# Performance work log

Hardware: AMD Instinct MI355X
Metric: run time of the kernel (lower is better)

Reference implementation:

```python
import jax, jax.numpy as jnp
import numpy as np

EPS = 1e-5   # torch F.layer_norm default eps
TOP_K = 20   # int(3*D^2 / (2*hr*N^2 + 10*D)) for D=768, N=196, hr=1.0
NUM_EXPERTS = 200  # 10 * TOP_K


def setup_inputs() -> dict:
    key = jax.random.key(0)
    ks = jax.random.split(key, 6)
    B, N, D = 32, 196, 768
    E, H = NUM_EXPERTS, 196  # H = int(N * hidden_ratio)
    s = 0.02
    return {
        "x": jax.random.normal(ks[0], (B, N, D), jnp.float32),
        "Wr": jax.random.normal(ks[1], (E, D), jnp.float32) * s,   # router.weight
        "W1": jax.random.normal(ks[2], (E, H, N), jnp.float32) * s,  # fc1.weight per expert
        "b1": jnp.zeros((E, H), jnp.float32),
        "W2": jax.random.normal(ks[3], (E, N, H), jnp.float32) * s,  # fc2.weight per expert
        "b2": jnp.zeros((E, N), jnp.float32),
        "Wo": jax.random.normal(ks[4], (D, D), jnp.float32) * s,     # out_proj.weight
        "bo": jnp.zeros((D,), jnp.float32),
    }


def reference(x, Wr, W1, b1, W2, b2, Wo, bo):
    B, N, D = x.shape
    E = Wr.shape[0]
    K = TOP_K

    # Router: per-sample routing on token-mean features
    logits = x.mean(axis=1) @ Wr.T                      # (B, E)
    probs = jax.nn.softmax(logits, axis=-1)             # (B, E)
    w, idx = jax.lax.top_k(probs, K)                    # (B, K) sorted desc, as torch.topk
    w = w / w.sum(axis=-1, keepdims=True)               # renormalize top-k weights

    # TokenMixer operates in (B, D, N) space: layernorm over tokens (no affine),
    # then fc1 (N->H), gelu(tanh), fc2 (H->N).
    xt = jnp.swapaxes(x, 1, 2)                          # (B, D, N)
    mu = xt.mean(axis=-1, keepdims=True)
    var = xt.var(axis=-1, keepdims=True)                # population var (matches F.layer_norm)
    z = (xt - mu) * jax.lax.rsqrt(var + EPS)            # (B, D, N)

    # Gather each sample's K expert weight matrices and batch the MLPs.
    W1g, b1g = W1[idx], b1[idx]                         # (B,K,H,N), (B,K,H)
    W2g, b2g = W2[idx], b2[idx]                         # (B,K,N,H), (B,K,N)

    h = jnp.einsum('bdn,bkhn->bkdh', z, W1g) + b1g[:, :, None, :]
    a = jax.nn.gelu(h, approximate=True)                # tanh-approx GELU
    o = jnp.einsum('bkdh,bknh->bkdn', a, W2g) + b2g[:, :, None, :]

    # Weighted combine over the K selected experts, back to (B, N, D)
    mix = jnp.einsum('bk,bkdn->bnd', w, o)

    out = mix @ Wo.T + bo                               # out_proj

    # Load-balancing aux loss (top-1 assignment fraction vs mean router prob)
    top1 = jax.nn.one_hot(idx[:, 0], E, dtype=probs.dtype)   # (B, E)
    aux = E * jnp.sum(probs.mean(axis=0) * top1.mean(axis=0))
    return out, aux
```

## Files before the change

kernel.cpp:

```cpp
#include <hip/hip_runtime.h>
#include <math.h>

constexpr int B  = 32;
constexpr int N  = 196;
constexpr int D  = 768;
constexpr int E  = 200;
constexpr int TK = 20;

constexpr int NGRP = 4;
constexpr int PRB  = 14336;
constexpr int EXB  = 114688;
constexpr int LK   = 40;

typedef __bf16 bf16x8 __attribute__((ext_vector_type(8)));
typedef __bf16 bf16x4 __attribute__((ext_vector_type(4)));
typedef float  f32x4  __attribute__((ext_vector_type(4)));
typedef long   longx2 __attribute__((ext_vector_type(2)));
typedef unsigned char uchar;

#define GLDS16(gp, lp)                                                        \
  __builtin_amdgcn_global_load_lds(                                           \
      (const __attribute__((address_space(1))) void*)(gp),                    \
      (__attribute__((address_space(3))) void*)(lp), 16, 0, 0)

#define WAITVM12  __builtin_amdgcn_s_waitcnt(0x0F7C)
#define WAITVM8   __builtin_amdgcn_s_waitcnt(0x0F78)
#define WAITVM0   __builtin_amdgcn_s_waitcnt(0x0F70)
#define WAITLGKM0 __builtin_amdgcn_s_waitcnt(0xC07F)
#define BAR       __builtin_amdgcn_s_barrier()

__device__ __forceinline__ float gelu_fast(float x) {
  float u = x * fmaf(x * x, 0.044715f, 1.0f);
  float e = exp2f(-2.3022084f * u);
  return x * __builtin_amdgcn_rcpf(1.0f + e);
}

__device__ __forceinline__ uchar f32_to_f8(float v) {
  return (uchar)(__builtin_amdgcn_cvt_pk_fp8_f32(v, v, 0, false) & 0xff);
}

__global__ __launch_bounds__(256) void k_ln(const float* __restrict__ x,
                                            uchar* __restrict__ zb,
                                            float* __restrict__ mu) {
  int b = blockIdx.x / 12, dt = blockIdx.x % 12;
  int d0 = dt * 64;
  int t = threadIdx.x;
  int q = t >> 6, d = t & 63;
  __shared__ float ps[256], pq[256];
  __shared__ float ms[64], rss[64];
  __shared__ alignas(16) uchar zt[64 * 256];

  for (int i = t; i < 1024; i += 256) ((uint4*)zt)[i] = (uint4){0, 0, 0, 0};

  const float* xp = x + ((size_t)b * N + q * 49) * D + d0 + d;
  float s = 0.f, sq = 0.f;
  #pragma unroll 7
  for (int n = 0; n < 49; ++n) {
    float v = xp[(size_t)n * D];
    s += v; sq += v * v;
  }
  ps[t] = s; pq[t] = sq;
  __syncthreads();
  if (t < 64) {
    float S = ps[t] + ps[t + 64] + ps[t + 128] + ps[t + 192];
    float Q = pq[t] + pq[t + 64] + pq[t + 128] + pq[t + 192];
    float m = S * (1.0f / N);
    float var = Q * (1.0f / N) - m * m;
    ms[t] = m; rss[t] = rsqrtf(var + 1e-5f);
    mu[(size_t)b * D + d0 + t] = m;
  }
  __syncthreads();
  float m = ms[d], r = rss[d];
  int dsw = (d >> 1) & 3;
  #pragma unroll 7
  for (int n = 0; n < 49; ++n) {
    float v = xp[(size_t)n * D];
    int tok = q * 49 + n;
    int qp = ((tok >> 3) & 3) ^ dsw;
    int off = d * 256 + (tok >> 6) * 64 + qp * 16 + ((tok >> 5) & 1) * 8 + (tok & 7);
    zt[off] = f32_to_f8((v - m) * r);
  }
  __syncthreads();
  #pragma unroll
  for (int pair = 0; pair < 4; ++pair) {
    uint4* dst = (uint4*)(zb + (((size_t)b * 4 + pair) * 768 + d0) * 64);
    dst[t] = ((const uint4*)zt)[(t >> 2) * 16 + pair * 4 + (t & 3)];
  }
}

__global__ __launch_bounds__(256) void k_convert(
    const float* __restrict__ W1, const float* __restrict__ W2,
    const float* __restrict__ Wo,
    uchar* __restrict__ Wf, __bf16* __restrict__ Wob) {
  int bx = blockIdx.x;
  int t = threadIdx.x;
  if (bx >= 400) {
    int i = (bx - 400) * 256 + t;
    float4 v = *(const float4*)&Wo[(size_t)i * 4];
    bf16x4 o = {(__bf16)v.x, (__bf16)v.y, (__bf16)v.z, (__bf16)v.w};
    *(bf16x4*)&Wob[(size_t)i * 4] = o;
    return;
  }
  int e = bx >> 1, mat = bx & 1;
  __shared__ alignas(16) uchar ls[224 * 256];
  for (int i = t; i < 3584; i += 256) ((uint4*)ls)[i] = (uint4){0, 0, 0, 0};
  __syncthreads();
  const float* src = (mat ? W2 : W1) + (size_t)e * 196 * 196;
  for (int i = t; i < 196 * 49; i += 256) {
    int r = i / 49, c4 = (i - r * 49) * 4;
    float4 v = *(const float4*)&src[(size_t)r * 196 + c4];
    int lo = __builtin_amdgcn_cvt_pk_fp8_f32(v.x, v.y, 0, false);
    unsigned int pk = (unsigned int)__builtin_amdgcn_cvt_pk_fp8_f32(v.z, v.w, lo, true);
    *(unsigned int*)&ls[r * 256 + c4] = pk;
  }
  __syncthreads();
  uchar* dst = Wf + (size_t)e * EXB + mat * 4 * PRB;
  for (int s = t; s < 3584; s += 256) {
    int p = s / 896, rem = s - p * 896;
    int col = rem >> 2, qp = rem & 3;
    int ql = qp ^ ((col >> 1) & 3);
    unsigned long lo = *(const unsigned long*)&ls[col * 256 + p * 64 + ql * 8];
    unsigned long hi = *(const unsigned long*)&ls[col * 256 + p * 64 + 32 + ql * 8];
    longx2 o; o[0] = (long)lo; o[1] = (long)hi;
    *(longx2*)&dst[(size_t)s * 16] = o;
  }
}

__global__ void k_router(const float* __restrict__ mu, const float* __restrict__ Wr,
                         float* __restrict__ probs, int* __restrict__ idxg,
                         float* __restrict__ wg) {
  int b = blockIdx.x;
  int t = threadIdx.x;
  __shared__ float smu[768];
  __shared__ float sp[E];
  __shared__ float smax, ssum;
  __shared__ float svals[TK];
  __shared__ int   sidx[TK];

  for (int i = t; i < 768; i += 256) smu[i] = mu[(size_t)b * D + i];
  __syncthreads();

  float logit = 0.f;
  if (t < E) {
    const float4* wr4 = (const float4*)(Wr + (size_t)t * D);
    const float4* m4  = (const float4*)smu;
    float acc = 0.f;
    #pragma unroll 4
    for (int i = 0; i < 192; ++i) {
      float4 w = wr4[i], m = m4[i];
      acc = fmaf(w.x, m.x, acc); acc = fmaf(w.y, m.y, acc);
      acc = fmaf(w.z, m.z, acc); acc = fmaf(w.w, m.w, acc);
    }
    logit = acc;
    sp[t] = acc;
  }
  __syncthreads();
  if (t == 0) {
    float mx = sp[0];
    for (int e = 1; e < E; ++e) mx = fmaxf(mx, sp[e]);
    smax = mx;
  }
  __syncthreads();
  if (t < E) sp[t] = expf(logit - smax);
  __syncthreads();
  if (t == 0) {
    float s = 0.f;
    for (int e = 0; e < E; ++e) s += sp[e];
    ssum = s;
  }
  __syncthreads();
  if (t < E) {
    sp[t] = sp[t] / ssum;
    probs[(size_t)b * E + t] = sp[t];
  }
  __syncthreads();

  for (int k = 0; k < TK; ++k) {
    if (t < 64) {
      float bv = -1e30f; int bi = 0;
      for (int e = t; e < E; e += 64) {
        float v = sp[e];
        if (v > bv) { bv = v; bi = e; }
      }
      #pragma unroll
      for (int off = 32; off > 0; off >>= 1) {
        float ov = __shfl_down(bv, off);
        int   oi = __shfl_down(bi, off);
        if (ov > bv || (ov == bv && oi < bi)) { bv = ov; bi = oi; }
      }
      if (t == 0) {
        svals[k] = bv; sidx[k] = bi;
        sp[bi] = -2e30f;
      }
    }
    __syncthreads();
  }
  if (t == 0) {
    float s = 0.f;
    for (int k = 0; k < TK; ++k) s += svals[k];
    float inv = 1.0f / s;
    for (int k = 0; k < TK; ++k) {
      wg[b * TK + k]   = svals[k] * inv;
      idxg[b * TK + k] = sidx[k];
    }
  }
}

__global__ __launch_bounds__(256, 2) void k_expert(
    const uchar* __restrict__ zb, const uchar* __restrict__ Wf,
    const float* __restrict__ b1, const float* __restrict__ b2,
    const int* __restrict__ idxg, const float* __restrict__ wg,
    __bf16* __restrict__ mixg) {
  __shared__ alignas(16) uchar pool[75776];
  __shared__ alignas(16) __bf16 b1s[5 * 196];
  __shared__ alignas(16) __bf16 b2s[5 * 196];
  __shared__ int   eidx_s[5];
  __shared__ float w_s[5];
  uchar* zs  = pool;
  uchar* at  = pool + 16384;
  uchar* wsb = pool + 32768;
  __bf16* tb = (__bf16*)pool;

  int xw = blockIdx.x & 7, rr_ = blockIdx.x >> 3;
  int j = rr_ / 12, dt = rr_ - j * 12;
  int gid = j * 8 + xw;
  int g = gid & 3, b = gid >> 2;
  int d0 = dt * 64;

  int t = threadIdx.x;
  int lane = t & 63, wave = t >> 6;
  int quad = lane >> 4, l16 = lane & 15;
  int wrow = (wave & 1) * 32;
  int wcol = (wave >> 1) * 112;
  int qp = quad ^ ((l16 >> 1) & 3);

  if (t < 5) {
    eidx_s[t] = idxg[b * TK + g * 5 + t];
    w_s[t]    = wg[b * TK + g * 5 + t];
  }
  for (int i = t; i < 980; i += 256) {
    int kk = i / 196, col = i - kk * 196;
    int ee = idxg[b * TK + g * 5 + kk];
    b1s[i] = (__bf16)b1[ee * 196 + col];
    b2s[i] = (__bf16)b2[ee * 196 + col];
  }
  *(unsigned long*)&at[3 * 4096 + (t >> 2) * 64 + (t & 3) * 16 + 8] = 0ul;
  __syncthreads();

  {
    const uchar* zbase = zb + ((size_t)b * 4 * 768 + d0) * 64;
    #pragma unroll
    for (int p = 0; p < 4; ++p)
      GLDS16(zbase + (size_t)p * (768 * 64) + t * 16, zs + p * 4096 + t * 16);
  }

  int s0 = t * 16, s1 = (t + 256) * 16, s2 = (t + 512) * 16;
  int s3 = ((t & 127) + 768) * 16;

  auto issue = [&](int qn) {
    int qq = qn > 39 ? 39 : qn;
    int kk2 = qq >> 3, rem = qq & 7;
    const uchar* src = Wf + (size_t)eidx_s[kk2] * EXB + rem * PRB;
    uchar* lb = wsb + (qn % 3) * PRB;
    GLDS16(src + s0, lb + s0);
    GLDS16(src + s1, lb + s1);
    GLDS16(src + s2, lb + s2);
    GLDS16(src + s3, lb + s3);
  };
  issue(0); issue(1); issue(2);

  WAITVM12;
  BAR;
  longx2 zf[4][2];
  #pragma unroll
  for (int p = 0; p < 4; ++p) {
    zf[p][0] = *(const longx2*)&zs[p * 4096 + (wrow + l16) * 64 + qp * 16];
    zf[p][1] = *(const longx2*)&zs[p * 4096 + (wrow + 16 + l16) * 64 + qp * 16];
  }

  f32x4 macc[14];
  #pragma unroll
  for (int i = 0; i < 14; ++i) macc[i] = (f32x4){0.f, 0.f, 0.f, 0.f};

  #pragma unroll 1
  for (int kk = 0; kk < 5; ++kk) {
    float wkv = w_s[kk];
    f32x4 hacc[14];
    #pragma unroll
    for (int i = 0; i < 14; ++i) hacc[i] = (f32x4){0.f, 0.f, 0.f, 0.f};

    #pragma unroll 1
    for (int p = 0; p < 4; ++p) {
      int q = kk * 8 + p;
      WAITVM8;
      BAR;
      const uchar* buf = wsb + (q % 3) * PRB;
      #pragma unroll
      for (int ct = 0; ct < 7; ++ct) {
        longx2 bf = *(const longx2*)&buf[(wcol + ct * 16 + l16) * 64 + qp * 16];
        hacc[ct]     = __builtin_amdgcn_mfma_f32_16x16x32_fp8_fp8(bf[0], zf[p][0][0], hacc[ct], 0, 0, 0);
        hacc[ct]     = __builtin_amdgcn_mfma_f32_16x16x32_fp8_fp8(bf[1], zf[p][0][1], hacc[ct], 0, 0, 0);
        hacc[7 + ct] = __builtin_amdgcn_mfma_f32_16x16x32_fp8_fp8(bf[0], zf[p][1][0], hacc[7 + ct], 0, 0, 0);
        hacc[7 + ct] = __builtin_amdgcn_mfma_f32_16x16x32_fp8_fp8(bf[1], zf[p][1][1], hacc[7 + ct], 0, 0, 0);
      }
      BAR;
      issue(q + 3);
    }

    #pragma unroll
    for (int ct = 0; ct < 7; ++ct) {
      int hb = wcol + ct * 16 + quad * 4;
      bool valid = hb < 196;
      unsigned pk0 = 0u, pk1 = 0u;
      if (valid) {
        bf16x4 b4 = *(const bf16x4*)&b1s[kk * 196 + hb];
        float bv0 = (float)b4[0], bv1 = (float)b4[1];
        float bv2 = (float)b4[2], bv3 = (float)b4[3];
        f32x4 h0 = hacc[ct], h1 = hacc[7 + ct];
        pk0 = (unsigned)__builtin_amdgcn_cvt_pk_fp8_f32(
                  gelu_fast(h0[0] + bv0) * wkv, gelu_fast(h0[1] + bv1) * wkv, 0, false);
        pk0 = (unsigned)__builtin_amdgcn_cvt_pk_fp8_f32(
                  gelu_fast(h0[2] + bv2) * wkv, gelu_fast(h0[3] + bv3) * wkv, (int)pk0, true);
        pk1 = (unsigned)__builtin_amdgcn_cvt_pk_fp8_f32(
                  gelu_fast(h1[0] + bv0) * wkv, gelu_fast(h1[1] + bv1) * wkv, 0, false);
        pk1 = (unsigned)__builtin_amdgcn_cvt_pk_fp8_f32(
                  gelu_fast(h1[2] + bv2) * wkv, gelu_fast(h1[3] + bv3) * wkv, (int)pk1, true);
      }
      int d0r = wrow + l16;
      int addr0 = (hb >> 6) * 4096 + d0r * 64 + ((((hb >> 3) & 3) ^ ((d0r >> 1) & 3)) << 4)
                + ((hb >> 5) & 1) * 8 + (quad & 1) * 4;
      *(unsigned*)&at[addr0]        = pk0;
      *(unsigned*)&at[addr0 + 1024] = pk1;
    }
    WAITLGKM0;

    #pragma unroll 1
    for (int p = 0; p < 4; ++p) {
      int q = kk * 8 + 4 + p;
      WAITVM8;
      BAR;
      const uchar* buf = wsb + (q % 3) * PRB;
      longx2 a0 = *(const longx2*)&at[p * 4096 + (wrow + l16) * 64 + qp * 16];
      longx2 a1 = *(const longx2*)&at[p * 4096 + (wrow + 16 + l16) * 64 + qp * 16];
      #pragma unroll
      for (int ct = 0; ct < 7; ++ct) {
        longx2 bf = *(const longx2*)&buf[(wcol + ct * 16 + l16) * 64 + qp * 16];
        macc[ct]     = __builtin_amdgcn_mfma_f32_16x16x32_fp8_fp8(a0[0], bf[0], macc[ct], 0, 0, 0);
        macc[ct]     = __builtin_amdgcn_mfma_f32_16x16x32_fp8_fp8(a0[1], bf[1], macc[ct], 0, 0, 0);
        macc[7 + ct] = __builtin_amdgcn_mfma_f32_16x16x32_fp8_fp8(a1[0], bf[0], macc[7 + ct], 0, 0, 0);
        macc[7 + ct] = __builtin_amdgcn_mfma_f32_16x16x32_fp8_fp8(a1[1], bf[1], macc[7 + ct], 0, 0, 0);
      }
      BAR;
      issue(q + 3);
    }
  }

  WAITVM0;
  BAR;
  #pragma unroll
  for (int ct = 0; ct < 7; ++ct) {
    int ncol = wcol + ct * 16 + l16;
    float bsum = 0.f;
    if (ncol < 196) {
      #pragma unroll
      for (int k5 = 0; k5 < 5; ++k5)
        bsum += w_s[k5] * (float)b2s[k5 * 196 + ncol];
    }
    #pragma unroll
    for (int rt = 0; rt < 2; ++rt) {
      f32x4 v = macc[rt * 7 + ct];
      bf16x4 o = {(__bf16)(v[0] + bsum), (__bf16)(v[1] + bsum),
                  (__bf16)(v[2] + bsum), (__bf16)(v[3] + bsum)};
      *(bf16x4*)&tb[ncol * 68 + wrow + rt * 16 + quad * 4] = o;
    }
  }
  __syncthreads();
  __bf16* mp = mixg + ((size_t)(g * B + b) * N) * D + d0;
  #pragma unroll
  for (int i = 0; i < 7; ++i) {
    int s = i * 256 + t;
    if (s < 1568) {
      int n = s >> 3, c = s & 7;
      const uint2* pa = (const uint2*)&tb[n * 68 + c * 8];
      uint2 v0 = pa[0], v1 = pa[1];
      uint4 v = {v0.x, v0.y, v1.x, v1.y};
      *(uint4*)&mp[(size_t)n * D + c * 8] = v;
    }
  }
}

__global__ __launch_bounds__(256, 2) void k_outproj(
    const __bf16* __restrict__ mixg, const __bf16* __restrict__ Wob,
    const float* __restrict__ bo, const float* __restrict__ probs,
    const int* __restrict__ idxg, float* __restrict__ out,
    float* __restrict__ out_aux) {
  __shared__ alignas(16) __bf16 As[64 * LK];
  __shared__ alignas(16) __bf16 Bs[256 * LK];
  const size_t GS = (size_t)B * N * D;

  int t = threadIdx.x;
  if (blockIdx.x == 0 && t < 32) {
    int top1 = idxg[t * TK];
    float s = 0.f;
    for (int bb = 0; bb < B; ++bb) s += probs[(size_t)bb * E + top1];
    #pragma unroll
    for (int off = 16; off > 0; off >>= 1) s += __shfl_down(s, off);
    if (t == 0) out_aux[0] = s * ((float)E / ((float)B * (float)B));
  }

  int m0 = (blockIdx.x % 98) * 64;
  int e0 = (blockIdx.x / 98) * 256;
  int lane = t & 63, wave = t >> 6;
  int quad = lane >> 4, l16 = lane & 15;
  int wrow = (wave & 1) * 32;
  int wcol = (wave >> 1) * 128;
  int arow = t >> 2, ach = t & 3;
  const __bf16* ap0 = mixg + (size_t)(m0 + arow) * D + ach * 8;

  f32x4 acc[16];
  #pragma unroll
  for (int i = 0; i < 16; ++i) acc[i] = (f32x4){0.f, 0.f, 0.f, 0.f};

  const uint4* wsrc = (const uint4*)Wob;
  #pragma unroll 1
  for (int c = 0; c < 24; ++c) {
    int k0 = c * 32;
    __syncthreads();
    {
      const __bf16* ap = ap0 + k0;
      bf16x8 g0 = *(const bf16x8*)(ap);
      bf16x8 g1 = *(const bf16x8*)(ap + GS);
      bf16x8 g2 = *(const bf16x8*)(ap + 2 * GS);
      bf16x8 g3 = *(const bf16x8*)(ap + 3 * GS);
      bf16x8 r;
      #pragma unroll
      for (int jj = 0; jj < 8; ++jj)
        r[jj] = (__bf16)((float)g0[jj] + (float)g1[jj] + (float)g2[jj] + (float)g3[jj]);
      *(bf16x8*)&As[arow * LK + ach * 8] = r;
    }
    for (int p = t; p < 1024; p += 256) {
      int rr = p >> 2, sub = p & 3;
      uint4 v = wsrc[(((size_t)(e0 + rr)) * D + k0) / 8 + sub];
      *(uint4*)&Bs[rr * LK + sub * 8] = v;
    }
    __syncthreads();
    bf16x8 a0 = *(const bf16x8*)&As[(wrow + l16) * LK + quad * 8];
    bf16x8 a1 = *(const bf16x8*)&As[(wrow + 16 + l16) * LK + quad * 8];
    #pragma unroll
    for (int ct = 0; ct < 8; ++ct) {
      bf16x8 bfr = *(const bf16x8*)&Bs[(wcol + ct * 16 + l16) * LK + quad * 8];
      acc[ct]     = __builtin_amdgcn_mfma_f32_16x16x32_bf16(a0, bfr, acc[ct], 0, 0, 0);
      acc[8 + ct] = __builtin_amdgcn_mfma_f32_16x16x32_bf16(a1, bfr, acc[8 + ct], 0, 0, 0);
    }
  }

  #pragma unroll
  for (int ct = 0; ct < 8; ++ct) {
    int e = e0 + wcol + ct * 16 + l16;
    float bov = bo[e];
    #pragma unroll
    for (int rt = 0; rt < 2; ++rt) {
      #pragma unroll
      for (int rx = 0; rx < 4; ++rx) {
        int m = m0 + wrow + rt * 16 + quad * 4 + rx;
        out[(size_t)m * D + e] = acc[rt * 8 + ct][rx] + bov;
      }
    }
  }
}

extern "C" void kernel_launch(void* const* d_in, const int* in_sizes, int n_in,
                              void* d_out, int out_size, void* d_ws, size_t ws_size,
                              hipStream_t stream) {
  const float* x  = (const float*)d_in[0];
  const float* Wr = (const float*)d_in[1];
  const float* W1 = (const float*)d_in[2];
  const float* b1 = (const float*)d_in[3];
  const float* W2 = (const float*)d_in[4];
  const float* b2 = (const float*)d_in[5];
  const float* Wo = (const float*)d_in[6];
  const float* bo = (const float*)d_in[7];
  float* out = (float*)d_out;

  char* p = (char*)d_ws;
  auto alloc = [&](size_t bytes) {
    char* r = p;
    p += (bytes + 255) & ~(size_t)255;
    return r;
  };
  uchar*  zb   = (uchar*)alloc((size_t)B * 4 * 768 * 64);
  float*  mu   = (float*)alloc((size_t)B * D * 4);
  uchar*  Wf   = (uchar*)alloc((size_t)E * EXB);
  __bf16* Wob  = (__bf16*)alloc((size_t)D * D * 2);
  __bf16* mixg = (__bf16*)alloc((size_t)NGRP * B * N * D * 2);
  float*  probs= (float*)alloc((size_t)B * E * 4);
  int*    idxg = (int*)alloc((size_t)B * TK * 4);
  float*  wg   = (float*)alloc((size_t)B * TK * 4);

  k_ln<<<dim3(B * 12), dim3(256), 0, stream>>>(x, zb, mu);
  k_convert<<<dim3(976), dim3(256), 0, stream>>>(W1, W2, Wo, Wf, Wob);
  k_router<<<dim3(B), dim3(256), 0, stream>>>(mu, Wr, probs, idxg, wg);
  k_expert<<<dim3(1536), dim3(256), 0, stream>>>(zb, Wf, b1, b2, idxg, wg, mixg);
  k_outproj<<<dim3(294), dim3(256), 0, stream>>>(mixg, Wob, bo, probs, idxg,
                                                 out, out + (size_t)B * N * D);
}
```

Before: 394.9 us.

## Fuse router into prep kernel, quad-buffer expert weights, shrink outproj tiles

Several changes land together. The layernorm kernel keeps the 49 x values in registers so x is not read twice. The router is folded into the weight-convert kernel as extra blocks, with wave-parallel dot products and shuffle reductions, which removes one launch and the serial single-thread loops. The expert kernel moves from triple to quad buffering by reusing the start of the shared pool, drops one barrier per step and raises wave priority around the MFMA bursts. The out-projection tile is halved to 32 rows so twice as many blocks run. The risks are a race on the reused pool region and a lower MFMA-to-load ratio in the out-projection.

Result: faster. 358.5 us (-9.2%).

```diff
diff --git a/kernel.cpp b/kernel.cpp
--- a/kernel.cpp
+++ b/kernel.cpp
@@ -53,11 +53,12 @@
   for (int i = t; i < 1024; i += 256) ((uint4*)zt)[i] = (uint4){0, 0, 0, 0};
 
   const float* xp = x + ((size_t)b * N + q * 49) * D + d0 + d;
+  float v[49];
   float s = 0.f, sq = 0.f;
-  #pragma unroll 7
+  #pragma unroll
   for (int n = 0; n < 49; ++n) {
-    float v = xp[(size_t)n * D];
-    s += v; sq += v * v;
+    v[n] = xp[(size_t)n * D];
+    s += v[n]; sq += v[n] * v[n];
   }
   ps[t] = s; pq[t] = sq;
   __syncthreads();
@@ -72,13 +73,12 @@
   __syncthreads();
   float m = ms[d], r = rss[d];
   int dsw = (d >> 1) & 3;
-  #pragma unroll 7
+  #pragma unroll
   for (int n = 0; n < 49; ++n) {
-    float v = xp[(size_t)n * D];
     int tok = q * 49 + n;
     int qp = ((tok >> 3) & 3) ^ dsw;
     int off = d * 256 + (tok >> 6) * 64 + qp * 16 + ((tok >> 5) & 1) * 8 + (tok & 7);
-    zt[off] = f32_to_f8((v - m) * r);
+    zt[off] = f32_to_f8((v[n] - m) * r);
   }
   __syncthreads();
   #pragma unroll
@@ -88,12 +88,99 @@
   }
 }
 
-__global__ __launch_bounds__(256) void k_convert(
+__global__ __launch_bounds__(256) void k_prep(
     const float* __restrict__ W1, const float* __restrict__ W2,
     const float* __restrict__ Wo,
-    uchar* __restrict__ Wf, __bf16* __restrict__ Wob) {
+    uchar* __restrict__ Wf, __bf16* __restrict__ Wob,
+    const float* __restrict__ mu, const float* __restrict__ Wr,
+    float* __restrict__ probs, int* __restrict__ idxg,
+    float* __restrict__ wg) {
   int bx = blockIdx.x;
   int t = threadIdx.x;
+  __shared__ alignas(16) uchar ls[224 * 256];
+  __shared__ float sp[E];
+  __shared__ float smax, ssum;
+  __shared__ float svals[TK];
+  __shared__ int   sidx[TK];
+
+  if (bx >= 976) {
+    int b = bx - 976;
+    int lane = t & 63, wave = t >> 6;
+    float* smu = (float*)ls;
+    for (int i = t; i < 768; i += 256) smu[i] = mu[(size_t)b * D + i];
+    __syncthreads();
+    const float4* m4 = (const float4*)smu;
+    #pragma unroll 1
+    for (int i = 0; i < 50; ++i) {
+      int e = wave * 50 + i;
+      const float4* wr4 = (const float4*)(Wr + (size_t)e * D);
+      float acc = 0.f;
+      #pragma unroll
+      for (int j = 0; j < 3; ++j) {
+        float4 w = wr4[lane + j * 64], mm = m4[lane + j * 64];
+        acc = fmaf(w.x, mm.x, acc); acc = fmaf(w.y, mm.y, acc);
+        acc = fmaf(w.z, mm.z, acc); acc = fmaf(w.w, mm.w, acc);
+      }
+      #pragma unroll
+      for (int off = 32; off > 0; off >>= 1) acc += __shfl_down(acc, off);
+      if (lane == 0) sp[e] = acc;
+    }
+    __syncthreads();
+    if (t < 64) {
+      float mx = -1e30f;
+      for (int e = t; e < E; e += 64) mx = fmaxf(mx, sp[e]);
+      #pragma unroll
+      for (int off = 32; off > 0; off >>= 1) mx = fmaxf(mx, __shfl_down(mx, off));
+      if (t == 0) smax = mx;
+    }
+    __syncthreads();
+    if (t < E) sp[t] = exp2f((sp[t] - smax) * 1.44269504f);
+    __syncthreads();
+    if (t < 64) {
+      float s = 0.f;
+      for (int e = t; e < E; e += 64) s += sp[e];
+      #pragma unroll
+      for (int off = 32; off > 0; off >>= 1) s += __shfl_down(s, off);
+      if (t == 0) ssum = s;
+    }
+    __syncthreads();
+    if (t < E) {
+      sp[t] = sp[t] / ssum;
+      probs[(size_t)b * E + t] = sp[t];
+    }
+    __syncthreads();
+    for (int k = 0; k < TK; ++k) {
+      if (t < 64) {
+        float bv = -1e30f; int bi = 0;
+        for (int e = t; e < E; e += 64) {
+          float v = sp[e];
+          if (v > bv) { bv = v; bi = e; }
+        }
+        #pragma unroll
+        for (int off = 32; off > 0; off >>= 1) {
+          float ov = __shfl_down(bv, off);
+          int   oi = __shfl_down(bi, off);
+          if (ov > bv || (ov == bv && oi < bi)) { bv = ov; bi = oi; }
+        }
+        if (t == 0) {
+          svals[k] = bv; sidx[k] = bi;
+          sp[bi] = -2e30f;
+        }
+      }
+      __syncthreads();
+    }
+    if (t == 0) {
+      float s = 0.f;
+      for (int k = 0; k < TK; ++k) s += svals[k];
+      float inv = 1.0f / s;
+      for (int k = 0; k < TK; ++k) {
+        wg[b * TK + k]   = svals[k] * inv;
+        idxg[b * TK + k] = sidx[k];
+      }
+    }
+    return;
+  }
+
   if (bx >= 400) {
     int i = (bx - 400) * 256 + t;
     float4 v = *(const float4*)&Wo[(size_t)i * 4];
@@ -102,7 +189,6 @@
     return;
   }
   int e = bx >> 1, mat = bx & 1;
-  __shared__ alignas(16) uchar ls[224 * 256];
   for (int i = t; i < 3584; i += 256) ((uint4*)ls)[i] = (uint4){0, 0, 0, 0};
   __syncthreads();
   const float* src = (mat ? W2 : W1) + (size_t)e * 196 * 196;
@@ -123,86 +209,6 @@
     unsigned long hi = *(const unsigned long*)&ls[col * 256 + p * 64 + 32 + ql * 8];
     longx2 o; o[0] = (long)lo; o[1] = (long)hi;
     *(longx2*)&dst[(size_t)s * 16] = o;
-  }
-}
-
-__global__ void k_router(const float* __restrict__ mu, const float* __restrict__ Wr,
-                         float* __restrict__ probs, int* __restrict__ idxg,
-                         float* __restrict__ wg) {
-  int b = blockIdx.x;
-  int t = threadIdx.x;
-  __shared__ float smu[768];
-  __shared__ float sp[E];
-  __shared__ float smax, ssum;
-  __shared__ float svals[TK];
-  __shared__ int   sidx[TK];
-
-  for (int i = t; i < 768; i += 256) smu[i] = mu[(size_t)b * D + i];
-  __syncthreads();
-
-  float logit = 0.f;
-  if (t < E) {
-    const float4* wr4 = (const float4*)(Wr + (size_t)t * D);
-    const float4* m4  = (const float4*)smu;
-    float acc = 0.f;
-    #pragma unroll 4
-    for (int i = 0; i < 192; ++i) {
-      float4 w = wr4[i], m = m4[i];
-      acc = fmaf(w.x, m.x, acc); acc = fmaf(w.y, m.y, acc);
-      acc = fmaf(w.z, m.z, acc); acc = fmaf(w.w, m.w, acc);
-    }
-    logit = acc;
-    sp[t] = acc;
-  }
-  __syncthreads();
-  if (t == 0) {
-    float mx = sp[0];
-    for (int e = 1; e < E; ++e) mx = fmaxf(mx, sp[e]);
-    smax = mx;
-  }
-  __syncthreads();
-  if (t < E) sp[t] = expf(logit - smax);
-  __syncthreads();
-  if (t == 0) {
-    float s = 0.f;
-    for (int e = 0; e < E; ++e) s += sp[e];
-    ssum = s;
-  }
-  __syncthreads();
-  if (t < E) {
-    sp[t] = sp[t] / ssum;
-    probs[(size_t)b * E + t] = sp[t];
-  }
-  __syncthreads();
-
-  for (int k = 0; k < TK; ++k) {
-    if (t < 64) {
-      float bv = -1e30f; int bi = 0;
-      for (int e = t; e < E; e += 64) {
-        float v = sp[e];
-        if (v > bv) { bv = v; bi = e; }
-      }
-      #pragma unroll
-      for (int off = 32; off > 0; off >>= 1) {
-        float ov = __shfl_down(bv, off);
-        int   oi = __shfl_down(bi, off);
-        if (ov > bv || (ov == bv && oi < bi)) { bv = ov; bi = oi; }
-      }
-      if (t == 0) {
-        svals[k] = bv; sidx[k] = bi;
-        sp[bi] = -2e30f;
-      }
-    }
-    __syncthreads();
-  }
-  if (t == 0) {
-    float s = 0.f;
-    for (int k = 0; k < TK; ++k) s += svals[k];
-    float inv = 1.0f / s;
-    for (int k = 0; k < TK; ++k) {
-      wg[b * TK + k]   = svals[k] * inv;
-      idxg[b * TK + k] = sidx[k];
-    }
   }
 }
 
@@ -261,7 +267,8 @@
     int qq = qn > 39 ? 39 : qn;
     int kk2 = qq >> 3, rem = qq & 7;
     const uchar* src = Wf + (size_t)eidx_s[kk2] * EXB + rem * PRB;
-    uchar* lb = wsb + (qn % 3) * PRB;
+    int bi = qn & 3;
+    uchar* lb = (bi == 3) ? pool : wsb + bi * PRB;
     GLDS16(src + s0, lb + s0);
     GLDS16(src + s1, lb + s1);
     GLDS16(src + s2, lb + s2);
@@ -294,7 +301,9 @@
       int q = kk * 8 + p;
       WAITVM8;
       BAR;
-      const uchar* buf = wsb + (q % 3) * PRB;
+      int bi = q & 3;
+      const uchar* buf = (bi == 3) ? pool : wsb + bi * PRB;
+      __builtin_amdgcn_s_setprio(1);
       #pragma unroll
       for (int ct = 0; ct < 7; ++ct) {
         longx2 bf = *(const longx2*)&buf[(wcol + ct * 16 + l16) * 64 + qp * 16];
@@ -303,7 +312,7 @@
         hacc[7 + ct] = __builtin_amdgcn_mfma_f32_16x16x32_fp8_fp8(bf[0], zf[p][1][0], hacc[7 + ct], 0, 0, 0);
         hacc[7 + ct] = __builtin_amdgcn_mfma_f32_16x16x32_fp8_fp8(bf[1], zf[p][1][1], hacc[7 + ct], 0, 0, 0);
       }
-      BAR;
+      __builtin_amdgcn_s_setprio(0);
       issue(q + 3);
     }
 
@@ -339,9 +348,11 @@
       int q = kk * 8 + 4 + p;
       WAITVM8;
       BAR;
-      const uchar* buf = wsb + (q % 3) * PRB;
+      int bi = q & 3;
+      const uchar* buf = (bi == 3) ? pool : wsb + bi * PRB;
       longx2 a0 = *(const longx2*)&at[p * 4096 + (wrow + l16) * 64 + qp * 16];
       longx2 a1 = *(const longx2*)&at[p * 4096 + (wrow + 16 + l16) * 64 + qp * 16];
+      __builtin_amdgcn_s_setprio(1);
       #pragma unroll
       for (int ct = 0; ct < 7; ++ct) {
         longx2 bf = *(const longx2*)&buf[(wcol + ct * 16 + l16) * 64 + qp * 16];
@@ -350,7 +361,7 @@
         macc[7 + ct] = __builtin_amdgcn_mfma_f32_16x16x32_fp8_fp8(a1[0], bf[0], macc[7 + ct], 0, 0, 0);
         macc[7 + ct] = __builtin_amdgcn_mfma_f32_16x16x32_fp8_fp8(a1[1], bf[1], macc[7 + ct], 0, 0, 0);
       }
-      BAR;
+      __builtin_amdgcn_s_setprio(0);
       issue(q + 3);
     }
   }
@@ -394,7 +405,7 @@
     const float* __restrict__ bo, const float* __restrict__ probs,
     const int* __restrict__ idxg, float* __restrict__ out,
     float* __restrict__ out_aux) {
-  __shared__ alignas(16) __bf16 As[64 * LK];
+  __shared__ alignas(16) __bf16 As[32 * LK];
   __shared__ alignas(16) __bf16 Bs[256 * LK];
   const size_t GS = (size_t)B * N * D;
 
@@ -408,25 +419,25 @@
     if (t == 0) out_aux[0] = s * ((float)E / ((float)B * (float)B));
   }
 
-  int m0 = (blockIdx.x % 98) * 64;
-  int e0 = (blockIdx.x / 98) * 256;
+  int m0 = (blockIdx.x % 196) * 32;
+  int e0 = (blockIdx.x / 196) * 256;
   int lane = t & 63, wave = t >> 6;
   int quad = lane >> 4, l16 = lane & 15;
-  int wrow = (wave & 1) * 32;
+  int wrow = (wave & 1) * 16;
   int wcol = (wave >> 1) * 128;
   int arow = t >> 2, ach = t & 3;
-  const __bf16* ap0 = mixg + (size_t)(m0 + arow) * D + ach * 8;
-
-  f32x4 acc[16];
-  #pragma unroll
-  for (int i = 0; i < 16; ++i) acc[i] = (f32x4){0.f, 0.f, 0.f, 0.f};
+  const __bf16* ap0 = mixg + (size_t)(m0 + (arow & 31)) * D + ach * 8;
+
+  f32x4 acc[8];
+  #pragma unroll
+  for (int i = 0; i < 8; ++i) acc[i] = (f32x4){0.f, 0.f, 0.f, 0.f};
 
   const uint4* wsrc = (const uint4*)Wob;
   #pragma unroll 1
   for (int c = 0; c < 24; ++c) {
     int k0 = c * 32;
     __syncthreads();
-    {
+    if (t < 128) {
       const __bf16* ap = ap0 + k0;
       bf16x8 g0 = *(const bf16x8*)(ap);
       bf16x8 g1 = *(const bf16x8*)(ap + GS);
@@ -445,12 +456,10 @@
     }
     __syncthreads();
     bf16x8 a0 = *(const bf16x8*)&As[(wrow + l16) * LK + quad * 8];
-    bf16x8 a1 = *(const bf16x8*)&As[(wrow + 16 + l16) * LK + quad * 8];
     #pragma unroll
     for (int ct = 0; ct < 8; ++ct) {
       bf16x8 bfr = *(const bf16x8*)&Bs[(wcol + ct * 16 + l16) * LK + quad * 8];
-      acc[ct]     = __builtin_amdgcn_mfma_f32_16x16x32_bf16(a0, bfr, acc[ct], 0, 0, 0);
-      acc[8 + ct] = __builtin_amdgcn_mfma_f32_16x16x32_bf16(a1, bfr, acc[8 + ct], 0, 0, 0);
+      acc[ct] = __builtin_amdgcn_mfma_f32_16x16x32_bf16(a0, bfr, acc[ct], 0, 0, 0);
     }
   }
 
@@ -459,12 +468,9 @@
     int e = e0 + wcol + ct * 16 + l16;
     float bov = bo[e];
     #pragma unroll
-    for (int rt = 0; rt < 2; ++rt) {
-      #pragma unroll
-      for (int rx = 0; rx < 4; ++rx) {
-        int m = m0 + wrow + rt * 16 + quad * 4 + rx;
-        out[(size_t)m * D + e] = acc[rt * 8 + ct][rx] + bov;
-      }
+    for (int rx = 0; rx < 4; ++rx) {
+      int m = m0 + wrow + quad * 4 + rx;
+      out[(size_t)m * D + e] = acc[ct][rx] + bov;
     }
   }
 }
@@ -498,9 +504,9 @@
   float*  wg   = (float*)alloc((size_t)B * TK * 4);
 
   k_ln<<<dim3(B * 12), dim3(256), 0, stream>>>(x, zb, mu);
-  k_convert<<<dim3(976), dim3(256), 0, stream>>>(W1, W2, Wo, Wf, Wob);
-  k_router<<<dim3(B), dim3(256), 0, stream>>>(mu, Wr, probs, idxg, wg);
+  k_prep<<<dim3(1008), dim3(256), 0, stream>>>(W1, W2, Wo, Wf, Wob,
+                                               mu, Wr, probs, idxg, wg);
   k_expert<<<dim3(1536), dim3(256), 0, stream>>>(zb, Wf, b1, b2, idxg, wg, mixg);
-  k_outproj<<<dim3(294), dim3(256), 0, stream>>>(mixg, Wob, bo, probs, idxg,
+  k_outproj<<<dim3(588), dim3(256), 0, stream>>>(mixg, Wob, bo, probs, idxg,
                                                  out, out + (size_t)B * N * D);
 }
```
